# Kernel optimization log

Measured on AMD Instinct MI355X. Metric: run time of the kernel, lower is better.

The kernel has to match this reference:

```python
import jax, jax.numpy as jnp
import numpy as np

N, E, IN, OUT, G = 100000, 800000, 64, 64, 250


def setup_inputs() -> dict:
    key = jax.random.key(0)
    ks = jax.random.split(key, 8)
    x = jax.random.normal(ks[0], (N, IN), dtype=jnp.float32)
    edge_index = jax.random.randint(ks[1], (2, E), 0, N, dtype=jnp.int32)
    edge_weight = jax.random.uniform(ks[2], (E,), dtype=jnp.float32)
    segment_ids = jnp.sort(jax.random.randint(ks[3], (N,), 0, G, dtype=jnp.int32))
    # GCNConv parameters (glorot-ish weights, zero bias as in PyG init)
    W_embed = jax.random.normal(ks[4], (IN, OUT), dtype=jnp.float32) / np.sqrt(IN)
    b_embed = jnp.zeros((OUT,), dtype=jnp.float32)
    W_pool = jax.random.normal(ks[5], (IN, 1), dtype=jnp.float32) / np.sqrt(IN)
    b_pool = jnp.zeros((1,), dtype=jnp.float32)
    return dict(x=x, W_embed=W_embed, b_embed=b_embed, W_pool=W_pool,
                b_pool=b_pool, edge_weight=edge_weight, edge_index=edge_index,
                segment_ids=segment_ids, num_segments=G)


def _gcn(x, W, b, row, col, ew, n):
    """PyG GCNConv: symmetric norm with self-loops already appended."""
    h = x @ W                                            # [N, F]
    deg = jax.ops.segment_sum(ew, col, num_segments=n)   # in-degree incl. self-loops
    dinv = jnp.where(deg > 0, jax.lax.rsqrt(deg), 0.0)
    norm = dinv[row] * ew * dinv[col]                    # [E+N]
    out = jax.ops.segment_sum(norm[:, None] * h[row], col, num_segments=n)
    return out + b


def reference(x, W_embed, b_embed, W_pool, b_pool, edge_weight,
              edge_index, segment_ids, num_segments):
    n = x.shape[0]
    loop = jnp.arange(n, dtype=edge_index.dtype)
    row = jnp.concatenate([edge_index[0], loop])         # add self-loops (w=1)
    col = jnp.concatenate([edge_index[1], loop])
    ew = jnp.concatenate([edge_weight, jnp.ones((n,), edge_weight.dtype)])

    embed = jax.nn.relu(_gcn(x, W_embed, b_embed, row, col, ew, n))  # [N, OUT]
    score = _gcn(x, W_pool, b_pool, row, col, ew, n)[:, 0]           # [N]

    # ragged per-graph softmax over node scores (stable)
    m = jax.ops.segment_max(score, segment_ids, num_segments=num_segments)
    e = jnp.exp(score - m[segment_ids])
    z = jax.ops.segment_sum(e, segment_ids, num_segments=num_segments)
    s = e / z[segment_ids]                               # [N]

    # softmax-weighted pooling of embeddings per graph -> [G, OUT]
    res = jax.ops.segment_sum(s[:, None] * embed, segment_ids,
                              num_segments=num_segments)
    return res
```

## Files before the change

### kernel.cpp

```cpp
#include <hip/hip_runtime.h>
#include <math.h>

#define NIN 64
#define CAP 16
#define GSEG 250
#define POOL_SPLIT 8
#define BND 256
#define CHUNK 2048
#define NBMAX 512

__device__ __forceinline__ float wave_reduce_sum(float v) {
    #pragma unroll
    for (int off = 32; off > 0; off >>= 1) v += __shfl_xor(v, off);
    return v;
}

__device__ __forceinline__ unsigned short f2bf(float f) {
    unsigned int u = __float_as_uint(f);
    u += 0x7FFFu + ((u >> 16) & 1u);
    return (unsigned short)(u >> 16);
}
__device__ __forceinline__ float bf2f(unsigned short h) {
    return __uint_as_float(((unsigned int)h) << 16);
}
__device__ __forceinline__ float bflo(unsigned int u) { return __uint_as_float(u << 16); }
__device__ __forceinline__ float bfhi(unsigned int u) { return __uint_as_float(u & 0xFFFF0000u); }
__device__ __forceinline__ unsigned int pack2bf(float lo, float hi) {
    return (unsigned int)f2bf(lo) | ((unsigned int)f2bf(hi) << 16);
}

__device__ __forceinline__ unsigned int f15enc(float w) {
    unsigned int u = __float_as_uint(w);
    u += 0x0FFFu + ((u >> 13) & 1u);
    int e5 = (int)(u >> 23) - 96;
    if (e5 <= 0) return 0u;
    unsigned int m = (u >> 13) & 0x3FFu;
    if (e5 > 31) { e5 = 31; m = 0x3FFu; }
    return ((unsigned int)e5 << 10) | m;
}
__device__ __forceinline__ float f15dec(unsigned int f) {
    if (f == 0u) return 0.0f;
    return __uint_as_float((((f >> 10) + 96u) << 23) | ((f & 0x3FFu) << 13));
}

__device__ __forceinline__ int wave_excl_scan_int(int x, int lane) {
    int inc = x;
    #pragma unroll
    for (int off = 1; off < 64; off <<= 1) {
        int y = __shfl_up(inc, off);
        if (lane >= off) inc += y;
    }
    return inc - x;
}

__device__ __forceinline__ void scan512_to_lds(const int* __restrict__ src,
                                               int* __restrict__ dst,
                                               int nb, int tid) {
    if (tid < 64) {
        int v[8];
        #pragma unroll
        for (int j = 0; j < 8; ++j) {
            int idx = tid * 8 + j;
            v[j] = (idx < nb) ? src[idx] : 0;
        }
        int loc = 0;
        #pragma unroll
        for (int j = 0; j < 8; ++j) loc += v[j];
        int ex = wave_excl_scan_int(loc, tid);
        int run = ex;
        #pragma unroll
        for (int j = 0; j < 8; ++j) {
            int idx = tid * 8 + j;
            if (idx < nb) { dst[idx] = run; run += v[j]; }
        }
    }
}

__global__ void __launch_bounds__(256)
k_prep(ushort4* __restrict__ x164, const float4* __restrict__ x4,
       float* __restrict__ out, int* __restrict__ gstart, int* __restrict__ gend,
       int* __restrict__ ovf_cnt, const int* __restrict__ col,
       int* __restrict__ ghist, int n, int e, int nb, int nblk) {
    __shared__ int h[NBMAX];
    int tid = threadIdx.x, blk = blockIdx.x;
    int i = blk * 256 + tid;
    int tot = n * (NIN / 4);
    if (i < tot) {
        float4 v = x4[i];
        ushort4 hh;
        hh.x = f2bf(v.x); hh.y = f2bf(v.y); hh.z = f2bf(v.z); hh.w = f2bf(v.w);
        x164[i] = hh;
    }
    if (i < GSEG * NIN) out[i] = 0.0f;
    if (i < GSEG) { gstart[i] = 0; gend[i] = 0; }
    if (i == 0) *ovf_cnt = 0;
    if (blk < nblk) {
        for (int j = tid; j < NBMAX; j += 256) h[j] = 0;
        __syncthreads();
        int base = blk * CHUNK;
        int end = base + CHUNK; if (end > e) end = e;
        for (int j = base + tid; j < end; j += 256) atomicAdd(&h[col[j] >> 8], 1);
        __syncthreads();
        for (int b = tid; b < nb; b += 256) ghist[blk * nb + b] = h[b];
    }
}

__global__ void k_scanA(int* __restrict__ ghist, int* __restrict__ btot,
                        const int* __restrict__ seg, int* __restrict__ gstart,
                        int* __restrict__ gend, int nblk, int nb, int n) {
    int b = blockIdx.x, lane = threadIdx.x;
    int v[8];
    #pragma unroll
    for (int j = 0; j < 8; ++j) {
        int idx = lane * 8 + j;
        v[j] = (idx < nblk) ? ghist[idx * nb + b] : 0;
    }
    int loc = 0;
    #pragma unroll
    for (int j = 0; j < 8; ++j) loc += v[j];
    int ex = wave_excl_scan_int(loc, lane);
    int run = ex;
    #pragma unroll
    for (int j = 0; j < 8; ++j) {
        int idx = lane * 8 + j;
        if (idx < nblk) { int t = v[j]; ghist[idx * nb + b] = run; run += t; }
    }
    if (lane == 63) btot[b] = ex + loc;

    int gsz = gridDim.x * 64;
    for (int i = b * 64 + lane; i < n; i += gsz) {
        int s = seg[i];
        if (i == 0 || seg[i - 1] != s) gstart[s] = i;
        if (i == n - 1 || seg[i + 1] != s) gend[s] = i + 1;
    }
}

__global__ void __launch_bounds__(256)
k_scatter(const int* __restrict__ row, const int* __restrict__ col,
          const float* __restrict__ ew, const int* __restrict__ ghist,
          const int* __restrict__ btot, uint2* __restrict__ bins,
          int e, int nb) {
    __shared__ int h[NBMAX];
    __shared__ int loff[NBMAX];
    __shared__ int gdst[NBMAX];
    __shared__ int bb[NBMAX];
    __shared__ uint2 recs[CHUNK];
    __shared__ unsigned short rb[CHUNK];
    int tid = threadIdx.x, blk = blockIdx.x;
    int base = blk * CHUNK;
    int end = base + CHUNK; if (end > e) end = e;
    int cnt = end - base;

    for (int i = tid; i < NBMAX; i += 256) h[i] = 0;
    __syncthreads();
    for (int i = base + tid; i < end; i += 256) atomicAdd(&h[col[i] >> 8], 1);
    __syncthreads();
    if (tid < 64) {
        int v[8];
        #pragma unroll
        for (int j = 0; j < 8; ++j) {
            int idx = tid * 8 + j;
            v[j] = (idx < nb) ? h[idx] : 0;
        }
        int loc = 0;
        #pragma unroll
        for (int j = 0; j < 8; ++j) loc += v[j];
        int ex = wave_excl_scan_int(loc, tid);
        int run = ex;
        #pragma unroll
        for (int j = 0; j < 8; ++j) {
            int idx = tid * 8 + j;
            if (idx < nb) { loff[idx] = run; run += v[j]; }
        }
    }
    scan512_to_lds(btot, bb, nb, tid);
    __syncthreads();
    for (int b = tid; b < nb; b += 256) gdst[b] = bb[b] + ghist[blk * nb + b];
    for (int i = tid; i < NBMAX; i += 256) h[i] = 0;
    __syncthreads();
    for (int i = base + tid; i < end; i += 256) {
        int c = col[i];
        int b = c >> 8;
        uint2 rec;
        rec.x = (unsigned int)row[i];
        rec.y = ((unsigned int)(c & (BND - 1)) << 15) | f15enc(ew[i]);
        int k = atomicAdd(&h[b], 1);
        int idx = loff[b] + k;
        recs[idx] = rec;
        rb[idx] = (unsigned short)b;
    }
    __syncthreads();
    for (int i = tid; i < cnt; i += 256) {
        int b = rb[i];
        bins[(size_t)gdst[b] + (i - loff[b])] = recs[i];
    }
}

__global__ void __launch_bounds__(256)
k_build(const uint2* __restrict__ bins, const int* __restrict__ btot,
        unsigned int* __restrict__ ell, float* __restrict__ deg,
        int* __restrict__ cnt, int2* __restrict__ ovf, int* __restrict__ ovf_cnt,
        float* __restrict__ aggf, int n, int nb) {
    int b = blockIdx.x;
    int c0 = b << 8;
    int nn = n - c0; if (nn > BND) nn = BND;
    __shared__ unsigned int tile[BND * CAP];
    __shared__ float sdeg[BND];
    __shared__ int scnt[BND];
    __shared__ int bb[NBMAX];
    __shared__ int ovl[BND];
    __shared__ int novloc;
    int tid = threadIdx.x;
    sdeg[tid] = 0.0f; scnt[tid] = 0;
    if (tid == 0) novloc = 0;
    for (int i = tid; i < BND * CAP; i += 256) tile[i] = 0u;
    scan512_to_lds(btot, bb, nb, tid);
    __syncthreads();
    int s0 = bb[b], tot = btot[b];
    for (int i = tid; i < tot; i += 256) {
        uint2 rec = bins[(size_t)s0 + i];
        int cl = (int)((rec.y >> 15) & (BND - 1));
        unsigned int w15 = rec.y & 0x7FFFu;
        atomicAdd(&sdeg[cl], f15dec(w15));
        int slot = atomicAdd(&scnt[cl], 1);
        unsigned int p = (rec.x << 15) | w15;
        if (slot < CAP) {
            tile[cl * CAP + slot] = p;
        } else {
            int oi = atomicAdd(ovf_cnt, 1);
            ovf[oi] = make_int2(c0 + cl, (int)p);
        }
    }
    __syncthreads();
    for (int i = tid; i < nn * CAP; i += 256)
        ell[(size_t)c0 * CAP + i] = tile[i];
    if (tid < nn) {
        deg[c0 + tid] = sdeg[tid] + 1.0f;
        cnt[c0 + tid] = scnt[tid];
        if (scnt[tid] > CAP) { int k = atomicAdd(&novloc, 1); ovl[k] = tid; }
    }
    __syncthreads();
    int nov = novloc;
    for (int k = 0; k < nov; ++k) {
        if (tid < NIN) aggf[(size_t)(c0 + ovl[k]) * NIN + tid] = 0.0f;
    }
}

__global__ void k_ovf(const int2* __restrict__ ovf, const int* __restrict__ ovf_cnt,
                      const float* __restrict__ deg, const ushort* __restrict__ x16,
                      float* __restrict__ aggf) {
    int nov = *ovf_cnt;
    int wid = (int)((blockIdx.x * (size_t)blockDim.x + threadIdx.x) >> 6);
    int lane = threadIdx.x & 63;
    int nw = (int)((gridDim.x * (size_t)blockDim.x) >> 6);
    for (int i = wid; i < nov; i += nw) {
        int2 ov = ovf[i];
        int c = ov.x;
        unsigned int p = (unsigned int)ov.y;
        int r = (int)(p >> 15);
        float w = f15dec(p & 0x7FFFu) * rsqrtf(deg[r]) * rsqrtf(deg[c]);
        atomicAdd(&aggf[(size_t)c * NIN + lane], w * bf2f(x16[(size_t)r * NIN + lane]));
    }
}

__global__ void __launch_bounds__(256)
k_gather(const ushort* __restrict__ x16, const float* __restrict__ deg,
         const int* __restrict__ cnt, const unsigned int* __restrict__ ell,
         const float* __restrict__ aggf, ushort* __restrict__ agg16,
         const float* __restrict__ Wp, const float* __restrict__ bp,
         float* __restrict__ score, int n) {
    int wid = (int)((blockIdx.x * (size_t)blockDim.x + threadIdx.x) >> 6);
    int lane = threadIdx.x & 63;
    int o = lane >> 3, l = lane & 7;
    int c0 = wid * 8;
    if (c0 >= n) return;
    int c = c0 + o;
    bool valid = c < n;
    int cc = valid ? c : (n - 1);

    int cr = cnt[cc];
    int m = valid ? (cr < CAP ? cr : CAP) : 0;
    float di = rsqrtf(deg[cc]);

    const uint2* ell2 = (const uint2*)ell;
    uint2 pe = ell2[(size_t)cc * 8 + l];
    int pr0 = (int)(pe.x >> 15);
    float pw0 = f15dec(pe.x & 0x7FFFu) * rsqrtf(deg[pr0]);
    int pr1 = (int)(pe.y >> 15);
    float pw1 = f15dec(pe.y & 0x7FFFu) * rsqrtf(deg[pr1]);

    const uint4* xr4 = (const uint4*)x16;
    uint4 xs = xr4[(size_t)cc * 8 + l];
    float a0 = di * bflo(xs.x), a1 = di * bfhi(xs.x);
    float a2 = di * bflo(xs.y), a3 = di * bfhi(xs.y);
    float a4 = di * bflo(xs.z), a5 = di * bfhi(xs.z);
    float a6 = di * bflo(xs.w), a7 = di * bfhi(xs.w);

    int base = lane & 56;
    #pragma unroll
    for (int k = 0; k < 8; ++k) {
        int rk = __shfl((k & 1) ? pr1 : pr0, base + (k >> 1));
        float wk = __shfl((k & 1) ? pw1 : pw0, base + (k >> 1));
        bool v = k < m;
        int r = v ? rk : 0;
        float w = v ? wk : 0.0f;
        uint4 xr = xr4[(size_t)r * 8 + l];
        a0 = fmaf(w, bflo(xr.x), a0); a1 = fmaf(w, bfhi(xr.x), a1);
        a2 = fmaf(w, bflo(xr.y), a2); a3 = fmaf(w, bfhi(xr.y), a3);
        a4 = fmaf(w, bflo(xr.z), a4); a5 = fmaf(w, bfhi(xr.z), a5);
        a6 = fmaf(w, bflo(xr.w), a6); a7 = fmaf(w, bfhi(xr.w), a7);
    }
    if (__any(m > 8)) {
        #pragma unroll
        for (int k = 8; k < CAP; ++k) {
            int rk = __shfl((k & 1) ? pr1 : pr0, base + (k >> 1));
            float wk = __shfl((k & 1) ? pw1 : pw0, base + (k >> 1));
            bool v = k < m;
            int r = v ? rk : 0;
            float w = v ? wk : 0.0f;
            uint4 xr = xr4[(size_t)r * 8 + l];
            a0 = fmaf(w, bflo(xr.x), a0); a1 = fmaf(w, bfhi(xr.x), a1);
            a2 = fmaf(w, bflo(xr.y), a2); a3 = fmaf(w, bfhi(xr.y), a3);
            a4 = fmaf(w, bflo(xr.z), a4); a5 = fmaf(w, bfhi(xr.z), a5);
            a6 = fmaf(w, bflo(xr.w), a6); a7 = fmaf(w, bfhi(xr.w), a7);
        }
    }
    a0 *= di; a1 *= di; a2 *= di; a3 *= di;
    a4 *= di; a5 *= di; a6 *= di; a7 *= di;

    if (valid && cr > CAP) {
        const float4* af4 = (const float4*)aggf;
        float4 f0 = af4[(size_t)cc * 16 + 2 * l];
        float4 f1 = af4[(size_t)cc * 16 + 2 * l + 1];
        a0 += f0.x; a1 += f0.y; a2 += f0.z; a3 += f0.w;
        a4 += f1.x; a5 += f1.y; a6 += f1.z; a7 += f1.w;
    }

    if (valid) {
        uint4 ho;
        ho.x = pack2bf(a0, a1); ho.y = pack2bf(a2, a3);
        ho.z = pack2bf(a4, a5); ho.w = pack2bf(a6, a7);
        ((uint4*)agg16)[(size_t)cc * 8 + l] = ho;
    }

    const float4* wp4 = (const float4*)Wp;
    float4 w0 = wp4[2 * l], w1 = wp4[2 * l + 1];
    float part = a0 * w0.x + a1 * w0.y + a2 * w0.z + a3 * w0.w
               + a4 * w1.x + a5 * w1.y + a6 * w1.z + a7 * w1.w;
    part += __shfl_xor(part, 1);
    part += __shfl_xor(part, 2);
    part += __shfl_xor(part, 4);
    if (l == 0 && valid) score[c] = part + bp[0];
}

#define WLOAD(i) float4 wq##i = make_float4(We[(4*(i)+0)*NIN+lane], We[(4*(i)+1)*NIN+lane], \
                                            We[(4*(i)+2)*NIN+lane], We[(4*(i)+3)*NIN+lane]);
#define WSTEP(i) { float4 av = *(const float4*)&als[wv][4*(i)]; \
    e0 = fmaf(av.x, wq##i.x, e0); e1 = fmaf(av.y, wq##i.y, e1); \
    e2 = fmaf(av.z, wq##i.z, e2); e3 = fmaf(av.w, wq##i.w, e3); }

__global__ void __launch_bounds__(256)
k_pool(const ushort* __restrict__ agg16, const float* __restrict__ score,
       const float* __restrict__ We, const float* __restrict__ be,
       const int* __restrict__ gstart, const int* __restrict__ gend,
       float* __restrict__ out) {
    int g = blockIdx.x / POOL_SPLIT;
    int p = blockIdx.x % POOL_SPLIT;
    int tid = threadIdx.x;
    int wv = tid >> 6, lane = tid & 63;
    int s = gstart[g], e = gend[g];

    __shared__ float red[4];
    __shared__ float bc;

    float mx = -3.402823466e38f;
    for (int i = s + tid; i < e; i += 256) mx = fmaxf(mx, score[i]);
    #pragma unroll
    for (int off = 32; off > 0; off >>= 1) mx = fmaxf(mx, __shfl_xor(mx, off));
    if (lane == 0) red[wv] = mx;
    __syncthreads();
    if (tid == 0) bc = fmaxf(fmaxf(red[0], red[1]), fmaxf(red[2], red[3]));
    __syncthreads();
    float m = bc;
    __syncthreads();

    float sm = 0.0f;
    for (int i = s + tid; i < e; i += 256) sm += __expf(score[i] - m);
    sm = wave_reduce_sum(sm);
    if (lane == 0) red[wv] = sm;
    __syncthreads();
    if (tid == 0) bc = red[0] + red[1] + red[2] + red[3];
    __syncthreads();
    float invz = (bc > 0.0f) ? 1.0f / bc : 0.0f;

    WLOAD(0) WLOAD(1) WLOAD(2) WLOAD(3) WLOAD(4) WLOAD(5) WLOAD(6) WLOAD(7)
    WLOAD(8) WLOAD(9) WLOAD(10) WLOAD(11) WLOAD(12) WLOAD(13) WLOAD(14) WLOAD(15)
    float bj = be[lane];

    __shared__ float als[4][NIN];
    __shared__ float part[4][NIN];

    const int stride = POOL_SPLIT * 4;
    int n = s + p * 4 + wv;
    float acc = 0.0f;

    float a_cur = 0.0f, sw_cur = 0.0f;
    if (n < e) {
        a_cur = bf2f(agg16[(size_t)n * NIN + lane]);
        sw_cur = __expf(score[n] - m) * invz;
    }
    while (n < e) {
        int nn = n + stride;
        bool vn = nn < e;
        int ni = vn ? nn : n;
        float a_nxt = bf2f(agg16[(size_t)ni * NIN + lane]);
        float sw_nxt = __expf(score[ni] - m) * invz;

        als[wv][lane] = a_cur;
        float e0 = bj, e1 = 0.0f, e2 = 0.0f, e3 = 0.0f;
        WSTEP(0) WSTEP(1) WSTEP(2) WSTEP(3) WSTEP(4) WSTEP(5) WSTEP(6) WSTEP(7)
        WSTEP(8) WSTEP(9) WSTEP(10) WSTEP(11) WSTEP(12) WSTEP(13) WSTEP(14) WSTEP(15)
        float emb = fmaxf(e0 + e1 + e2 + e3, 0.0f);
        acc = fmaf(sw_cur, emb, acc);

        a_cur = a_nxt; sw_cur = sw_nxt;
        n = nn;
    }
    part[wv][lane] = acc;
    __syncthreads();
    if (wv == 0) {
        float r = part[0][lane] + part[1][lane] + part[2][lane] + part[3][lane];
        atomicAdd(&out[(size_t)g * NIN + lane], r);
    }
}

extern "C" void kernel_launch(void* const* d_in, const int* in_sizes, int n_in,
                              void* d_out, int out_size, void* d_ws, size_t ws_size,
                              hipStream_t stream) {
    const float* x  = (const float*)d_in[0];
    const float* We = (const float*)d_in[1];
    const float* be = (const float*)d_in[2];
    const float* Wp = (const float*)d_in[3];
    const float* bp = (const float*)d_in[4];
    const float* ew = (const float*)d_in[5];
    const int* eidx = (const int*)d_in[6];
    const int* seg  = (const int*)d_in[7];

    int N = in_sizes[0] / NIN;
    int E = in_sizes[5];
    const int* row = eidx;
    const int* col = eidx + E;
    int nb   = (N + BND - 1) / BND;
    int nblk = (E + CHUNK - 1) / CHUNK;

    char* w = (char*)d_ws;
    auto alloc = [&](size_t bytes) {
        char* p = w;
        w += (bytes + 255) & ~(size_t)255;
        return p;
    };
    float*          aggf    = (float*)alloc((size_t)N * NIN * sizeof(float));
    unsigned short* x16     = (unsigned short*)alloc((size_t)N * NIN * sizeof(short));
    unsigned short* agg16   = (unsigned short*)alloc((size_t)N * NIN * sizeof(short));
    float*          deg     = (float*)alloc((size_t)N * sizeof(float));
    int*            cnt     = (int*)  alloc((size_t)N * sizeof(int));
    unsigned int*   ell     = (unsigned int*)alloc((size_t)N * CAP * sizeof(unsigned int));
    uint2*          bins    = (uint2*)alloc((size_t)E * sizeof(uint2));
    int*            ghist   = (int*)  alloc((size_t)nblk * nb * sizeof(int));
    int*            btot    = (int*)  alloc((size_t)nb * sizeof(int));
    int2*           ovf     = (int2*) alloc((size_t)(E / 4) * sizeof(int2));
    int*            ovf_cnt = (int*)  alloc(256);
    float*          score   = (float*)alloc((size_t)N * sizeof(float));
    int*            gstart  = (int*)  alloc(GSEG * sizeof(int));
    int*            gend    = (int*)  alloc(GSEG * sizeof(int));
    float* out = (float*)d_out;

    int b = 256;
    int g_prep   = (N * (NIN / 4) + b - 1) / b;
    int nwaves   = (N + 7) / 8;
    int g_gather = (nwaves + 3) / 4;

    k_prep<<<g_prep, b, 0, stream>>>((ushort4*)x16, (const float4*)x, out, gstart,
                                     gend, ovf_cnt, col, ghist, N, E, nb, nblk);
    k_scanA<<<nb, 64, 0, stream>>>(ghist, btot, seg, gstart, gend, nblk, nb, N);
    k_scatter<<<nblk, b, 0, stream>>>(row, col, ew, ghist, btot, bins, E, nb);
    k_build<<<nb, b, 0, stream>>>(bins, btot, ell, deg, cnt, ovf, ovf_cnt, aggf, N, nb);
    k_ovf<<<64, b, 0, stream>>>(ovf, ovf_cnt, deg, x16, aggf);
    k_gather<<<g_gather, b, 0, stream>>>(x16, deg, cnt, ell, aggf, agg16, Wp, bp, score, N);
    k_pool<<<GSEG * POOL_SPLIT, b, 0, stream>>>(agg16, score, We, be, gstart, gend, out);
}
```

Measured before the change: 89.08 us.

## Fuse bucket build, overflow handling and gather into one LDS-tiled kernel

Merges k_build, k_ovf and k_gather into a single kernel, k_bg. It keeps each bucket's ELL tile and overflow edges in LDS and gathers directly from there, so the global ELL, count and fp32 overflow buffers are no longer needed. Degree is now computed with global atomics inside the scan kernel, and the symmetric normalisation is folded into the edge weight during scatter. Buckets shrink to 128 nodes to fit the larger tile. In exchange there are fewer gather blocks, more serial work per block, and overflow edges beyond 256 per bucket would be silently dropped.

```diff
diff --git a/kernel.cpp b/kernel.cpp
--- a/kernel.cpp
+++ b/kernel.cpp
@@ -5,9 +5,12 @@
 #define CAP 16
 #define GSEG 250
 #define POOL_SPLIT 8
-#define BND 256
+#define BND 128
+#define BSH 7
 #define CHUNK 2048
-#define NBMAX 512
+#define NBMAX 1024
+#define OVRMAX 256
+#define TS 17
 
 __device__ __forceinline__ float wave_reduce_sum(float v) {
     #pragma unroll
@@ -53,24 +56,23 @@
     return inc - x;
 }
 
-__device__ __forceinline__ void scan512_to_lds(const int* __restrict__ src,
-                                               int* __restrict__ dst,
-                                               int nb, int tid) {
+__device__ __forceinline__ void scan_btot(const int* __restrict__ src,
+                                          int* dst, int nb, int tid) {
     if (tid < 64) {
-        int v[8];
-        #pragma unroll
-        for (int j = 0; j < 8; ++j) {
-            int idx = tid * 8 + j;
+        int v[16];
+        #pragma unroll
+        for (int j = 0; j < 16; ++j) {
+            int idx = tid * 16 + j;
             v[j] = (idx < nb) ? src[idx] : 0;
         }
         int loc = 0;
         #pragma unroll
-        for (int j = 0; j < 8; ++j) loc += v[j];
+        for (int j = 0; j < 16; ++j) loc += v[j];
         int ex = wave_excl_scan_int(loc, tid);
         int run = ex;
         #pragma unroll
-        for (int j = 0; j < 8; ++j) {
-            int idx = tid * 8 + j;
+        for (int j = 0; j < 16; ++j) {
+            int idx = tid * 16 + j;
             if (idx < nb) { dst[idx] = run; run += v[j]; }
         }
     }
@@ -79,7 +81,7 @@
 __global__ void __launch_bounds__(256)
 k_prep(ushort4* __restrict__ x164, const float4* __restrict__ x4,
        float* __restrict__ out, int* __restrict__ gstart, int* __restrict__ gend,
-       int* __restrict__ ovf_cnt, const int* __restrict__ col,
+       float* __restrict__ deg, const int* __restrict__ col,
        int* __restrict__ ghist, int n, int e, int nb, int nblk) {
     __shared__ int h[NBMAX];
     int tid = threadIdx.x, blk = blockIdx.x;
@@ -91,44 +93,51 @@
         hh.x = f2bf(v.x); hh.y = f2bf(v.y); hh.z = f2bf(v.z); hh.w = f2bf(v.w);
         x164[i] = hh;
     }
+    if (i < n) deg[i] = 0.0f;
     if (i < GSEG * NIN) out[i] = 0.0f;
     if (i < GSEG) { gstart[i] = 0; gend[i] = 0; }
-    if (i == 0) *ovf_cnt = 0;
     if (blk < nblk) {
         for (int j = tid; j < NBMAX; j += 256) h[j] = 0;
         __syncthreads();
         int base = blk * CHUNK;
         int end = base + CHUNK; if (end > e) end = e;
-        for (int j = base + tid; j < end; j += 256) atomicAdd(&h[col[j] >> 8], 1);
+        for (int j = base + tid; j < end; j += 256) atomicAdd(&h[col[j] >> BSH], 1);
         __syncthreads();
         for (int b = tid; b < nb; b += 256) ghist[blk * nb + b] = h[b];
     }
 }
 
-__global__ void k_scanA(int* __restrict__ ghist, int* __restrict__ btot,
-                        const int* __restrict__ seg, int* __restrict__ gstart,
-                        int* __restrict__ gend, int nblk, int nb, int n) {
-    int b = blockIdx.x, lane = threadIdx.x;
-    int v[8];
-    #pragma unroll
-    for (int j = 0; j < 8; ++j) {
-        int idx = lane * 8 + j;
-        v[j] = (idx < nblk) ? ghist[idx * nb + b] : 0;
-    }
-    int loc = 0;
-    #pragma unroll
-    for (int j = 0; j < 8; ++j) loc += v[j];
-    int ex = wave_excl_scan_int(loc, lane);
-    int run = ex;
-    #pragma unroll
-    for (int j = 0; j < 8; ++j) {
-        int idx = lane * 8 + j;
-        if (idx < nblk) { int t = v[j]; ghist[idx * nb + b] = run; run += t; }
-    }
-    if (lane == 63) btot[b] = ex + loc;
-
-    int gsz = gridDim.x * 64;
-    for (int i = b * 64 + lane; i < n; i += gsz) {
+__global__ void __launch_bounds__(256)
+k_scanA(int* __restrict__ ghist, int* __restrict__ btot,
+        const int* __restrict__ seg, int* __restrict__ gstart,
+        int* __restrict__ gend, const int* __restrict__ col,
+        const float* __restrict__ ew, float* __restrict__ deg,
+        int nblk, int nb, int n, int e) {
+    int tid = threadIdx.x;
+    int b = blockIdx.x;
+    if (tid < 64) {
+        int lane = tid;
+        int v[8];
+        #pragma unroll
+        for (int j = 0; j < 8; ++j) {
+            int idx = lane * 8 + j;
+            v[j] = (idx < nblk) ? ghist[idx * nb + b] : 0;
+        }
+        int loc = 0;
+        #pragma unroll
+        for (int j = 0; j < 8; ++j) loc += v[j];
+        int ex = wave_excl_scan_int(loc, lane);
+        int run = ex;
+        #pragma unroll
+        for (int j = 0; j < 8; ++j) {
+            int idx = lane * 8 + j;
+            if (idx < nblk) { int t = v[j]; ghist[idx * nb + b] = run; run += t; }
+        }
+        if (lane == 63) btot[b] = ex + loc;
+    }
+    int gsz = gridDim.x * 256;
+    for (int i = b * 256 + tid; i < e; i += gsz) atomicAdd(&deg[col[i]], ew[i]);
+    for (int i = b * 256 + tid; i < n; i += gsz) {
         int s = seg[i];
         if (i == 0 || seg[i - 1] != s) gstart[s] = i;
         if (i == n - 1 || seg[i + 1] != s) gend[s] = i + 1;
@@ -137,9 +146,9 @@
 
 __global__ void __launch_bounds__(256)
 k_scatter(const int* __restrict__ row, const int* __restrict__ col,
-          const float* __restrict__ ew, const int* __restrict__ ghist,
-          const int* __restrict__ btot, uint2* __restrict__ bins,
-          int e, int nb) {
+          const float* __restrict__ ew, const float* __restrict__ deg,
+          const int* __restrict__ ghist, const int* __restrict__ btot,
+          uint2* __restrict__ bins, int e, int nb) {
     __shared__ int h[NBMAX];
     __shared__ int loff[NBMAX];
     __shared__ int gdst[NBMAX];
@@ -149,170 +158,125 @@
     int tid = threadIdx.x, blk = blockIdx.x;
     int base = blk * CHUNK;
     int end = base + CHUNK; if (end > e) end = e;
-    int cnt = end - base;
+    int cntc = end - base;
 
     for (int i = tid; i < NBMAX; i += 256) h[i] = 0;
     __syncthreads();
-    for (int i = base + tid; i < end; i += 256) atomicAdd(&h[col[i] >> 8], 1);
+    for (int i = base + tid; i < end; i += 256) atomicAdd(&h[col[i] >> BSH], 1);
     __syncthreads();
     if (tid < 64) {
-        int v[8];
-        #pragma unroll
-        for (int j = 0; j < 8; ++j) {
-            int idx = tid * 8 + j;
+        int v[16];
+        #pragma unroll
+        for (int j = 0; j < 16; ++j) {
+            int idx = tid * 16 + j;
             v[j] = (idx < nb) ? h[idx] : 0;
         }
         int loc = 0;
         #pragma unroll
-        for (int j = 0; j < 8; ++j) loc += v[j];
+        for (int j = 0; j < 16; ++j) loc += v[j];
         int ex = wave_excl_scan_int(loc, tid);
         int run = ex;
         #pragma unroll
-        for (int j = 0; j < 8; ++j) {
-            int idx = tid * 8 + j;
+        for (int j = 0; j < 16; ++j) {
+            int idx = tid * 16 + j;
             if (idx < nb) { loff[idx] = run; run += v[j]; }
         }
     }
-    scan512_to_lds(btot, bb, nb, tid);
+    scan_btot(btot, bb, nb, tid);
     __syncthreads();
     for (int b = tid; b < nb; b += 256) gdst[b] = bb[b] + ghist[blk * nb + b];
     for (int i = tid; i < NBMAX; i += 256) h[i] = 0;
     __syncthreads();
     for (int i = base + tid; i < end; i += 256) {
-        int c = col[i];
-        int b = c >> 8;
+        int c = col[i], r = row[i];
+        int b = c >> BSH;
+        float w = ew[i] * rsqrtf(deg[r] + 1.0f) * rsqrtf(deg[c] + 1.0f);
         uint2 rec;
-        rec.x = (unsigned int)row[i];
-        rec.y = ((unsigned int)(c & (BND - 1)) << 15) | f15enc(ew[i]);
+        rec.x = (unsigned int)r;
+        rec.y = ((unsigned int)(c & (BND - 1)) << 15) | f15enc(w);
         int k = atomicAdd(&h[b], 1);
         int idx = loff[b] + k;
         recs[idx] = rec;
         rb[idx] = (unsigned short)b;
     }
     __syncthreads();
-    for (int i = tid; i < cnt; i += 256) {
+    for (int i = tid; i < cntc; i += 256) {
         int b = rb[i];
         bins[(size_t)gdst[b] + (i - loff[b])] = recs[i];
     }
 }
 
 __global__ void __launch_bounds__(256)
-k_build(const uint2* __restrict__ bins, const int* __restrict__ btot,
-        unsigned int* __restrict__ ell, float* __restrict__ deg,
-        int* __restrict__ cnt, int2* __restrict__ ovf, int* __restrict__ ovf_cnt,
-        float* __restrict__ aggf, int n, int nb) {
-    int b = blockIdx.x;
-    int c0 = b << 8;
-    int nn = n - c0; if (nn > BND) nn = BND;
-    __shared__ unsigned int tile[BND * CAP];
-    __shared__ float sdeg[BND];
+k_bg(const uint2* __restrict__ bins, const int* __restrict__ btot,
+     const float* __restrict__ deg, const ushort* __restrict__ x16,
+     ushort* __restrict__ agg16, const float* __restrict__ Wp,
+     const float* __restrict__ bp, float* __restrict__ score, int n, int nb) {
+    __shared__ unsigned int tile[BND * TS];
     __shared__ int scnt[BND];
     __shared__ int bb[NBMAX];
-    __shared__ int ovl[BND];
-    __shared__ int novloc;
+    __shared__ int ovr_cl[OVRMAX];
+    __shared__ unsigned int ovr_rec[OVRMAX];
+    __shared__ int ovn;
     int tid = threadIdx.x;
-    sdeg[tid] = 0.0f; scnt[tid] = 0;
-    if (tid == 0) novloc = 0;
-    for (int i = tid; i < BND * CAP; i += 256) tile[i] = 0u;
-    scan512_to_lds(btot, bb, nb, tid);
-    __syncthreads();
+    int b = blockIdx.x;
+    int c0 = b << BSH;
+
+    if (tid < BND) scnt[tid] = 0;
+    if (tid == 0) ovn = 0;
+    scan_btot(btot, bb, nb, tid);
+    __syncthreads();
+
     int s0 = bb[b], tot = btot[b];
     for (int i = tid; i < tot; i += 256) {
         uint2 rec = bins[(size_t)s0 + i];
         int cl = (int)((rec.y >> 15) & (BND - 1));
-        unsigned int w15 = rec.y & 0x7FFFu;
-        atomicAdd(&sdeg[cl], f15dec(w15));
+        unsigned int p = (rec.x << 15) | (rec.y & 0x7FFFu);
         int slot = atomicAdd(&scnt[cl], 1);
-        unsigned int p = (rec.x << 15) | w15;
         if (slot < CAP) {
-            tile[cl * CAP + slot] = p;
+            tile[cl * TS + slot] = p;
         } else {
-            int oi = atomicAdd(ovf_cnt, 1);
-            ovf[oi] = make_int2(c0 + cl, (int)p);
-        }
-    }
-    __syncthreads();
-    for (int i = tid; i < nn * CAP; i += 256)
-        ell[(size_t)c0 * CAP + i] = tile[i];
-    if (tid < nn) {
-        deg[c0 + tid] = sdeg[tid] + 1.0f;
-        cnt[c0 + tid] = scnt[tid];
-        if (scnt[tid] > CAP) { int k = atomicAdd(&novloc, 1); ovl[k] = tid; }
-    }
-    __syncthreads();
-    int nov = novloc;
-    for (int k = 0; k < nov; ++k) {
-        if (tid < NIN) aggf[(size_t)(c0 + ovl[k]) * NIN + tid] = 0.0f;
-    }
-}
-
-__global__ void k_ovf(const int2* __restrict__ ovf, const int* __restrict__ ovf_cnt,
-                      const float* __restrict__ deg, const ushort* __restrict__ x16,
-                      float* __restrict__ aggf) {
-    int nov = *ovf_cnt;
-    int wid = (int)((blockIdx.x * (size_t)blockDim.x + threadIdx.x) >> 6);
-    int lane = threadIdx.x & 63;
-    int nw = (int)((gridDim.x * (size_t)blockDim.x) >> 6);
-    for (int i = wid; i < nov; i += nw) {
-        int2 ov = ovf[i];
-        int c = ov.x;
-        unsigned int p = (unsigned int)ov.y;
-        int r = (int)(p >> 15);
-        float w = f15dec(p & 0x7FFFu) * rsqrtf(deg[r]) * rsqrtf(deg[c]);
-        atomicAdd(&aggf[(size_t)c * NIN + lane], w * bf2f(x16[(size_t)r * NIN + lane]));
-    }
-}
-
-__global__ void __launch_bounds__(256)
-k_gather(const ushort* __restrict__ x16, const float* __restrict__ deg,
-         const int* __restrict__ cnt, const unsigned int* __restrict__ ell,
-         const float* __restrict__ aggf, ushort* __restrict__ agg16,
-         const float* __restrict__ Wp, const float* __restrict__ bp,
-         float* __restrict__ score, int n) {
-    int wid = (int)((blockIdx.x * (size_t)blockDim.x + threadIdx.x) >> 6);
-    int lane = threadIdx.x & 63;
+            int oi = atomicAdd(&ovn, 1);
+            if (oi < OVRMAX) { ovr_cl[oi] = cl; ovr_rec[oi] = p; }
+        }
+    }
+    __syncthreads();
+
+    int lane = tid & 63, wv = tid >> 6;
     int o = lane >> 3, l = lane & 7;
-    int c0 = wid * 8;
-    if (c0 >= n) return;
-    int c = c0 + o;
-    bool valid = c < n;
-    int cc = valid ? c : (n - 1);
-
-    int cr = cnt[cc];
-    int m = valid ? (cr < CAP ? cr : CAP) : 0;
-    float di = rsqrtf(deg[cc]);
-
-    const uint2* ell2 = (const uint2*)ell;
-    uint2 pe = ell2[(size_t)cc * 8 + l];
-    int pr0 = (int)(pe.x >> 15);
-    float pw0 = f15dec(pe.x & 0x7FFFu) * rsqrtf(deg[pr0]);
-    int pr1 = (int)(pe.y >> 15);
-    float pw1 = f15dec(pe.y & 0x7FFFu) * rsqrtf(deg[pr1]);
-
+    const float4* wp4 = (const float4*)Wp;
+    float4 w0 = wp4[2 * l], w1 = wp4[2 * l + 1];
+    float bp0 = bp[0];
     const uint4* xr4 = (const uint4*)x16;
-    uint4 xs = xr4[(size_t)cc * 8 + l];
-    float a0 = di * bflo(xs.x), a1 = di * bfhi(xs.x);
-    float a2 = di * bflo(xs.y), a3 = di * bfhi(xs.y);
-    float a4 = di * bflo(xs.z), a5 = di * bfhi(xs.z);
-    float a6 = di * bflo(xs.w), a7 = di * bfhi(xs.w);
-
-    int base = lane & 56;
+    int nov = ovn;
+
     #pragma unroll
-    for (int k = 0; k < 8; ++k) {
-        int rk = __shfl((k & 1) ? pr1 : pr0, base + (k >> 1));
-        float wk = __shfl((k & 1) ? pw1 : pw0, base + (k >> 1));
-        bool v = k < m;
-        int r = v ? rk : 0;
-        float w = v ? wk : 0.0f;
-        uint4 xr = xr4[(size_t)r * 8 + l];
-        a0 = fmaf(w, bflo(xr.x), a0); a1 = fmaf(w, bfhi(xr.x), a1);
-        a2 = fmaf(w, bflo(xr.y), a2); a3 = fmaf(w, bfhi(xr.y), a3);
-        a4 = fmaf(w, bflo(xr.z), a4); a5 = fmaf(w, bfhi(xr.z), a5);
-        a6 = fmaf(w, bflo(xr.w), a6); a7 = fmaf(w, bfhi(xr.w), a7);
-    }
-    if (__any(m > 8)) {
-        #pragma unroll
-        for (int k = 8; k < CAP; ++k) {
+    for (int it = 0; it < BND / 32; ++it) {
+        int bl = it * 32 + wv * 8;
+        int nl = bl + o;
+        int c = c0 + nl;
+        bool valid = c < n;
+        int cc = valid ? c : (n - 1);
+        int cr = scnt[nl];
+        int m = valid ? (cr < CAP ? cr : CAP) : 0;
+        float di = rsqrtf(deg[cc] + 1.0f);
+
+        unsigned int u0 = tile[nl * TS + 2 * l];
+        unsigned int u1 = tile[nl * TS + 2 * l + 1];
+        int pr0 = (int)(u0 >> 15);
+        float pw0 = f15dec(u0 & 0x7FFFu);
+        int pr1 = (int)(u1 >> 15);
+        float pw1 = f15dec(u1 & 0x7FFFu);
+
+        uint4 xs = xr4[(size_t)cc * 8 + l];
+        float s2 = di * di;
+        float a0 = s2 * bflo(xs.x), a1 = s2 * bfhi(xs.x);
+        float a2 = s2 * bflo(xs.y), a3 = s2 * bfhi(xs.y);
+        float a4 = s2 * bflo(xs.z), a5 = s2 * bfhi(xs.z);
+        float a6 = s2 * bflo(xs.w), a7 = s2 * bfhi(xs.w);
+
+        int base = lane & 56;
+        #pragma unroll
+        for (int k = 0; k < 8; ++k) {
             int rk = __shfl((k & 1) ? pr1 : pr0, base + (k >> 1));
             float wk = __shfl((k & 1) ? pw1 : pw0, base + (k >> 1));
             bool v = k < m;
@@ -324,33 +288,49 @@
             a4 = fmaf(w, bflo(xr.z), a4); a5 = fmaf(w, bfhi(xr.z), a5);
             a6 = fmaf(w, bflo(xr.w), a6); a7 = fmaf(w, bfhi(xr.w), a7);
         }
-    }
-    a0 *= di; a1 *= di; a2 *= di; a3 *= di;
-    a4 *= di; a5 *= di; a6 *= di; a7 *= di;
-
-    if (valid && cr > CAP) {
-        const float4* af4 = (const float4*)aggf;
-        float4 f0 = af4[(size_t)cc * 16 + 2 * l];
-        float4 f1 = af4[(size_t)cc * 16 + 2 * l + 1];
-        a0 += f0.x; a1 += f0.y; a2 += f0.z; a3 += f0.w;
-        a4 += f1.x; a5 += f1.y; a6 += f1.z; a7 += f1.w;
-    }
-
-    if (valid) {
-        uint4 ho;
-        ho.x = pack2bf(a0, a1); ho.y = pack2bf(a2, a3);
-        ho.z = pack2bf(a4, a5); ho.w = pack2bf(a6, a7);
-        ((uint4*)agg16)[(size_t)cc * 8 + l] = ho;
-    }
-
-    const float4* wp4 = (const float4*)Wp;
-    float4 w0 = wp4[2 * l], w1 = wp4[2 * l + 1];
-    float part = a0 * w0.x + a1 * w0.y + a2 * w0.z + a3 * w0.w
-               + a4 * w1.x + a5 * w1.y + a6 * w1.z + a7 * w1.w;
-    part += __shfl_xor(part, 1);
-    part += __shfl_xor(part, 2);
-    part += __shfl_xor(part, 4);
-    if (l == 0 && valid) score[c] = part + bp[0];
+        if (__any(m > 8)) {
+            #pragma unroll
+            for (int k = 8; k < CAP; ++k) {
+                int rk = __shfl((k & 1) ? pr1 : pr0, base + (k >> 1));
+                float wk = __shfl((k & 1) ? pw1 : pw0, base + (k >> 1));
+                bool v = k < m;
+                int r = v ? rk : 0;
+                float w = v ? wk : 0.0f;
+                uint4 xr = xr4[(size_t)r * 8 + l];
+                a0 = fmaf(w, bflo(xr.x), a0); a1 = fmaf(w, bfhi(xr.x), a1);
+                a2 = fmaf(w, bflo(xr.y), a2); a3 = fmaf(w, bfhi(xr.y), a3);
+                a4 = fmaf(w, bflo(xr.z), a4); a5 = fmaf(w, bfhi(xr.z), a5);
+                a6 = fmaf(w, bflo(xr.w), a6); a7 = fmaf(w, bfhi(xr.w), a7);
+            }
+        }
+        for (int i = 0; i < nov; ++i) {
+            int cl = ovr_cl[i];
+            if (cl >= bl && cl < bl + 8) {
+                unsigned int rec = ovr_rec[i];
+                int r = (int)(rec >> 15);
+                float wvv = f15dec(rec & 0x7FFFu);
+                float wm = (cl == nl) ? wvv : 0.0f;
+                uint4 xr = xr4[(size_t)r * 8 + l];
+                a0 = fmaf(wm, bflo(xr.x), a0); a1 = fmaf(wm, bfhi(xr.x), a1);
+                a2 = fmaf(wm, bflo(xr.y), a2); a3 = fmaf(wm, bfhi(xr.y), a3);
+                a4 = fmaf(wm, bflo(xr.z), a4); a5 = fmaf(wm, bfhi(xr.z), a5);
+                a6 = fmaf(wm, bflo(xr.w), a6); a7 = fmaf(wm, bfhi(xr.w), a7);
+            }
+        }
+
+        if (valid) {
+            uint4 ho;
+            ho.x = pack2bf(a0, a1); ho.y = pack2bf(a2, a3);
+            ho.z = pack2bf(a4, a5); ho.w = pack2bf(a6, a7);
+            ((uint4*)agg16)[(size_t)cc * 8 + l] = ho;
+        }
+        float part = a0 * w0.x + a1 * w0.y + a2 * w0.z + a3 * w0.w
+                   + a4 * w1.x + a5 * w1.y + a6 * w1.z + a7 * w1.w;
+        part += __shfl_xor(part, 1);
+        part += __shfl_xor(part, 2);
+        part += __shfl_xor(part, 4);
+        if (l == 0 && valid) score[c] = part + bp0;
+    }
 }
 
 #define WLOAD(i) float4 wq##i = make_float4(We[(4*(i)+0)*NIN+lane], We[(4*(i)+1)*NIN+lane], \
@@ -459,33 +439,25 @@
         w += (bytes + 255) & ~(size_t)255;
         return p;
     };
-    float*          aggf    = (float*)alloc((size_t)N * NIN * sizeof(float));
-    unsigned short* x16     = (unsigned short*)alloc((size_t)N * NIN * sizeof(short));
-    unsigned short* agg16   = (unsigned short*)alloc((size_t)N * NIN * sizeof(short));
-    float*          deg     = (float*)alloc((size_t)N * sizeof(float));
-    int*            cnt     = (int*)  alloc((size_t)N * sizeof(int));
-    unsigned int*   ell     = (unsigned int*)alloc((size_t)N * CAP * sizeof(unsigned int));
-    uint2*          bins    = (uint2*)alloc((size_t)E * sizeof(uint2));
-    int*            ghist   = (int*)  alloc((size_t)nblk * nb * sizeof(int));
-    int*            btot    = (int*)  alloc((size_t)nb * sizeof(int));
-    int2*           ovf     = (int2*) alloc((size_t)(E / 4) * sizeof(int2));
-    int*            ovf_cnt = (int*)  alloc(256);
-    float*          score   = (float*)alloc((size_t)N * sizeof(float));
-    int*            gstart  = (int*)  alloc(GSEG * sizeof(int));
-    int*            gend    = (int*)  alloc(GSEG * sizeof(int));
+    unsigned short* x16    = (unsigned short*)alloc((size_t)N * NIN * sizeof(short));
+    unsigned short* agg16  = (unsigned short*)alloc((size_t)N * NIN * sizeof(short));
+    float*          deg    = (float*)alloc((size_t)N * sizeof(float));
+    uint2*          bins   = (uint2*)alloc((size_t)E * sizeof(uint2));
+    int*            ghist  = (int*)  alloc((size_t)nblk * nb * sizeof(int));
+    int*            btot   = (int*)  alloc((size_t)nb * sizeof(int));
+    float*          score  = (float*)alloc((size_t)N * sizeof(float));
+    int*            gstart = (int*)  alloc(GSEG * sizeof(int));
+    int*            gend   = (int*)  alloc(GSEG * sizeof(int));
     float* out = (float*)d_out;
 
     int b = 256;
-    int g_prep   = (N * (NIN / 4) + b - 1) / b;
-    int nwaves   = (N + 7) / 8;
-    int g_gather = (nwaves + 3) / 4;
+    int g_prep = (N * (NIN / 4) + b - 1) / b;
 
     k_prep<<<g_prep, b, 0, stream>>>((ushort4*)x16, (const float4*)x, out, gstart,
-                                     gend, ovf_cnt, col, ghist, N, E, nb, nblk);
-    k_scanA<<<nb, 64, 0, stream>>>(ghist, btot, seg, gstart, gend, nblk, nb, N);
-    k_scatter<<<nblk, b, 0, stream>>>(row, col, ew, ghist, btot, bins, E, nb);
-    k_build<<<nb, b, 0, stream>>>(bins, btot, ell, deg, cnt, ovf, ovf_cnt, aggf, N, nb);
-    k_ovf<<<64, b, 0, stream>>>(ovf, ovf_cnt, deg, x16, aggf);
-    k_gather<<<g_gather, b, 0, stream>>>(x16, deg, cnt, ell, aggf, agg16, Wp, bp, score, N);
+                                     gend, deg, col, ghist, N, E, nb, nblk);
+    k_scanA<<<nb, b, 0, stream>>>(ghist, btot, seg, gstart, gend, col, ew, deg,
+                                  nblk, nb, N, E);
+    k_scatter<<<nblk, b, 0, stream>>>(row, col, ew, deg, ghist, btot, bins, E, nb);
+    k_bg<<<nb, b, 0, stream>>>(bins, btot, deg, x16, agg16, Wp, bp, score, N, nb);
     k_pool<<<GSEG * POOL_SPLIT, b, 0, stream>>>(agg16, score, We, be, gstart, gend, out);
 }
```

Measured after the change: 129.3 us. 1.45x slower.

## Fold overflow edge handling into gather via per-bucket overflow lists

Applied to the files above, without the earlier changes.

Edges beyond each node's ELL capacity are no longer pushed to a global list by global atomics. k_build now keeps them in a small shared-memory list per 256-node bucket and writes that list out. k_gather then walks its bucket's overflow entries and accumulates the matching ones directly. This removes the k_ovf launch, the float aggregation buffer with its global atomic adds, and the extra read in gather. The cost is that every gather wave scans all overflow entries of its bucket. Overflow beyond 128 entries per bucket is silently dropped, which risks wrong results on skewed degree distributions.

```diff
diff --git a/kernel.cpp b/kernel.cpp
--- a/kernel.cpp
+++ b/kernel.cpp
@@ -8,6 +8,7 @@
 #define BND 256
 #define CHUNK 2048
 #define NBMAX 512
+#define OVR 128
 
 __device__ __forceinline__ float wave_reduce_sum(float v) {
     #pragma unroll
@@ -53,9 +54,8 @@
     return inc - x;
 }
 
-__device__ __forceinline__ void scan512_to_lds(const int* __restrict__ src,
-                                               int* __restrict__ dst,
-                                               int nb, int tid) {
+__device__ __forceinline__ void scan_btot(const int* __restrict__ src,
+                                          int* dst, int nb, int tid) {
     if (tid < 64) {
         int v[8];
         #pragma unroll
@@ -79,8 +79,8 @@
 __global__ void __launch_bounds__(256)
 k_prep(ushort4* __restrict__ x164, const float4* __restrict__ x4,
        float* __restrict__ out, int* __restrict__ gstart, int* __restrict__ gend,
-       int* __restrict__ ovf_cnt, const int* __restrict__ col,
-       int* __restrict__ ghist, int n, int e, int nb, int nblk) {
+       const int* __restrict__ col, int* __restrict__ ghist,
+       int n, int e, int nb, int nblk) {
     __shared__ int h[NBMAX];
     int tid = threadIdx.x, blk = blockIdx.x;
     int i = blk * 256 + tid;
@@ -93,7 +93,6 @@
     }
     if (i < GSEG * NIN) out[i] = 0.0f;
     if (i < GSEG) { gstart[i] = 0; gend[i] = 0; }
-    if (i == 0) *ovf_cnt = 0;
     if (blk < nblk) {
         for (int j = tid; j < NBMAX; j += 256) h[j] = 0;
         __syncthreads();
@@ -149,7 +148,7 @@
     int tid = threadIdx.x, blk = blockIdx.x;
     int base = blk * CHUNK;
     int end = base + CHUNK; if (end > e) end = e;
-    int cnt = end - base;
+    int cntc = end - base;
 
     for (int i = tid; i < NBMAX; i += 256) h[i] = 0;
     __syncthreads();
@@ -173,16 +172,16 @@
             if (idx < nb) { loff[idx] = run; run += v[j]; }
         }
     }
-    scan512_to_lds(btot, bb, nb, tid);
+    scan_btot(btot, bb, nb, tid);
     __syncthreads();
     for (int b = tid; b < nb; b += 256) gdst[b] = bb[b] + ghist[blk * nb + b];
     for (int i = tid; i < NBMAX; i += 256) h[i] = 0;
     __syncthreads();
     for (int i = base + tid; i < end; i += 256) {
-        int c = col[i];
+        int c = col[i], r = row[i];
         int b = c >> 8;
         uint2 rec;
-        rec.x = (unsigned int)row[i];
+        rec.x = (unsigned int)r;
         rec.y = ((unsigned int)(c & (BND - 1)) << 15) | f15enc(ew[i]);
         int k = atomicAdd(&h[b], 1);
         int idx = loff[b] + k;
@@ -190,7 +189,7 @@
         rb[idx] = (unsigned short)b;
     }
     __syncthreads();
-    for (int i = tid; i < cnt; i += 256) {
+    for (int i = tid; i < cntc; i += 256) {
         int b = rb[i];
         bins[(size_t)gdst[b] + (i - loff[b])] = recs[i];
     }
@@ -199,22 +198,22 @@
 __global__ void __launch_bounds__(256)
 k_build(const uint2* __restrict__ bins, const int* __restrict__ btot,
         unsigned int* __restrict__ ell, float* __restrict__ deg,
-        int* __restrict__ cnt, int2* __restrict__ ovf, int* __restrict__ ovf_cnt,
-        float* __restrict__ aggf, int n, int nb) {
-    int b = blockIdx.x;
-    int c0 = b << 8;
-    int nn = n - c0; if (nn > BND) nn = BND;
+        int* __restrict__ cnt, int* __restrict__ ovfc, int2* __restrict__ ovfe,
+        int n, int nb) {
     __shared__ unsigned int tile[BND * CAP];
     __shared__ float sdeg[BND];
     __shared__ int scnt[BND];
     __shared__ int bb[NBMAX];
-    __shared__ int ovl[BND];
-    __shared__ int novloc;
+    __shared__ int2 sovf[OVR];
+    __shared__ int sovn;
     int tid = threadIdx.x;
+    int b = blockIdx.x;
+    int c0 = b << 8;
+    int nn = n - c0; if (nn > BND) nn = BND;
     sdeg[tid] = 0.0f; scnt[tid] = 0;
-    if (tid == 0) novloc = 0;
+    if (tid == 0) sovn = 0;
     for (int i = tid; i < BND * CAP; i += 256) tile[i] = 0u;
-    scan512_to_lds(btot, bb, nb, tid);
+    scan_btot(btot, bb, nb, tid);
     __syncthreads();
     int s0 = bb[b], tot = btot[b];
     for (int i = tid; i < tot; i += 256) {
@@ -227,8 +226,8 @@
         if (slot < CAP) {
             tile[cl * CAP + slot] = p;
         } else {
-            int oi = atomicAdd(ovf_cnt, 1);
-            ovf[oi] = make_int2(c0 + cl, (int)p);
+            int oi = atomicAdd(&sovn, 1);
+            if (oi < OVR) sovf[oi] = make_int2(((int)rec.x << 8) | cl, (int)w15);
         }
     }
     __syncthreads();
@@ -237,46 +236,25 @@
     if (tid < nn) {
         deg[c0 + tid] = sdeg[tid] + 1.0f;
         cnt[c0 + tid] = scnt[tid];
-        if (scnt[tid] > CAP) { int k = atomicAdd(&novloc, 1); ovl[k] = tid; }
-    }
-    __syncthreads();
-    int nov = novloc;
-    for (int k = 0; k < nov; ++k) {
-        if (tid < NIN) aggf[(size_t)(c0 + ovl[k]) * NIN + tid] = 0.0f;
-    }
-}
-
-__global__ void k_ovf(const int2* __restrict__ ovf, const int* __restrict__ ovf_cnt,
-                      const float* __restrict__ deg, const ushort* __restrict__ x16,
-                      float* __restrict__ aggf) {
-    int nov = *ovf_cnt;
-    int wid = (int)((blockIdx.x * (size_t)blockDim.x + threadIdx.x) >> 6);
-    int lane = threadIdx.x & 63;
-    int nw = (int)((gridDim.x * (size_t)blockDim.x) >> 6);
-    for (int i = wid; i < nov; i += nw) {
-        int2 ov = ovf[i];
-        int c = ov.x;
-        unsigned int p = (unsigned int)ov.y;
-        int r = (int)(p >> 15);
-        float w = f15dec(p & 0x7FFFu) * rsqrtf(deg[r]) * rsqrtf(deg[c]);
-        atomicAdd(&aggf[(size_t)c * NIN + lane], w * bf2f(x16[(size_t)r * NIN + lane]));
-    }
+    }
+    int nov = sovn < OVR ? sovn : OVR;
+    if (tid == 0) ovfc[b] = nov;
+    for (int i = tid; i < nov; i += 256) ovfe[(size_t)b * OVR + i] = sovf[i];
 }
 
 __global__ void __launch_bounds__(256)
 k_gather(const ushort* __restrict__ x16, const float* __restrict__ deg,
          const int* __restrict__ cnt, const unsigned int* __restrict__ ell,
-         const float* __restrict__ aggf, ushort* __restrict__ agg16,
-         const float* __restrict__ Wp, const float* __restrict__ bp,
-         float* __restrict__ score, int n) {
-    int wid = (int)((blockIdx.x * (size_t)blockDim.x + threadIdx.x) >> 6);
-    int lane = threadIdx.x & 63;
+         const int* __restrict__ ovfc, const int2* __restrict__ ovfe,
+         ushort* __restrict__ agg16, const float* __restrict__ Wp,
+         const float* __restrict__ bp, float* __restrict__ score, int n) {
+    int tid = threadIdx.x, blk = blockIdx.x;
+    int lane = tid & 63, wv = tid >> 6;
     int o = lane >> 3, l = lane & 7;
-    int c0 = wid * 8;
-    if (c0 >= n) return;
-    int c = c0 + o;
+    int c = blk * 32 + wv * 8 + o;
     bool valid = c < n;
     int cc = valid ? c : (n - 1);
+    int b = blk >> 3;
 
     int cr = cnt[cc];
     int m = valid ? (cr < CAP ? cr : CAP) : 0;
@@ -325,16 +303,22 @@
             a6 = fmaf(w, bflo(xr.w), a6); a7 = fmaf(w, bfhi(xr.w), a7);
         }
     }
+    int novb = ovfc[b];
+    int nl = cc & (BND - 1);
+    for (int i = 0; i < novb; ++i) {
+        int2 ent = ovfe[(size_t)b * OVR + i];
+        int cl = ent.x & (BND - 1);
+        int r = ent.x >> 8;
+        bool mine = (cl == nl) && valid;
+        float wm = mine ? f15dec((unsigned int)ent.y) * rsqrtf(deg[r]) : 0.0f;
+        uint4 xr = xr4[(size_t)r * 8 + l];
+        a0 = fmaf(wm, bflo(xr.x), a0); a1 = fmaf(wm, bfhi(xr.x), a1);
+        a2 = fmaf(wm, bflo(xr.y), a2); a3 = fmaf(wm, bfhi(xr.y), a3);
+        a4 = fmaf(wm, bflo(xr.z), a4); a5 = fmaf(wm, bfhi(xr.z), a5);
+        a6 = fmaf(wm, bflo(xr.w), a6); a7 = fmaf(wm, bfhi(xr.w), a7);
+    }
     a0 *= di; a1 *= di; a2 *= di; a3 *= di;
     a4 *= di; a5 *= di; a6 *= di; a7 *= di;
-
-    if (valid && cr > CAP) {
-        const float4* af4 = (const float4*)aggf;
-        float4 f0 = af4[(size_t)cc * 16 + 2 * l];
-        float4 f1 = af4[(size_t)cc * 16 + 2 * l + 1];
-        a0 += f0.x; a1 += f0.y; a2 += f0.z; a3 += f0.w;
-        a4 += f1.x; a5 += f1.y; a6 += f1.z; a7 += f1.w;
-    }
 
     if (valid) {
         uint4 ho;
@@ -342,7 +326,6 @@
         ho.z = pack2bf(a4, a5); ho.w = pack2bf(a6, a7);
         ((uint4*)agg16)[(size_t)cc * 8 + l] = ho;
     }
-
     const float4* wp4 = (const float4*)Wp;
     float4 w0 = wp4[2 * l], w1 = wp4[2 * l + 1];
     float part = a0 * w0.x + a1 * w0.y + a2 * w0.z + a3 * w0.w
@@ -459,33 +442,31 @@
         w += (bytes + 255) & ~(size_t)255;
         return p;
     };
-    float*          aggf    = (float*)alloc((size_t)N * NIN * sizeof(float));
-    unsigned short* x16     = (unsigned short*)alloc((size_t)N * NIN * sizeof(short));
-    unsigned short* agg16   = (unsigned short*)alloc((size_t)N * NIN * sizeof(short));
-    float*          deg     = (float*)alloc((size_t)N * sizeof(float));
-    int*            cnt     = (int*)  alloc((size_t)N * sizeof(int));
-    unsigned int*   ell     = (unsigned int*)alloc((size_t)N * CAP * sizeof(unsigned int));
-    uint2*          bins    = (uint2*)alloc((size_t)E * sizeof(uint2));
-    int*            ghist   = (int*)  alloc((size_t)nblk * nb * sizeof(int));
-    int*            btot    = (int*)  alloc((size_t)nb * sizeof(int));
-    int2*           ovf     = (int2*) alloc((size_t)(E / 4) * sizeof(int2));
-    int*            ovf_cnt = (int*)  alloc(256);
-    float*          score   = (float*)alloc((size_t)N * sizeof(float));
-    int*            gstart  = (int*)  alloc(GSEG * sizeof(int));
-    int*            gend    = (int*)  alloc(GSEG * sizeof(int));
+    unsigned short* x16    = (unsigned short*)alloc((size_t)N * NIN * sizeof(short));
+    unsigned short* agg16  = (unsigned short*)alloc((size_t)N * NIN * sizeof(short));
+    float*          deg    = (float*)alloc((size_t)N * sizeof(float));
+    int*            cnt    = (int*)  alloc((size_t)N * sizeof(int));
+    unsigned int*   ell    = (unsigned int*)alloc((size_t)N * CAP * sizeof(unsigned int));
+    uint2*          bins   = (uint2*)alloc((size_t)E * sizeof(uint2));
+    int*            ghist  = (int*)  alloc((size_t)nblk * nb * sizeof(int));
+    int*            btot   = (int*)  alloc((size_t)nb * sizeof(int));
+    int*            ovfc   = (int*)  alloc((size_t)nb * sizeof(int));
+    int2*           ovfe   = (int2*) alloc((size_t)nb * OVR * sizeof(int2));
+    float*          score  = (float*)alloc((size_t)N * sizeof(float));
+    int*            gstart = (int*)  alloc(GSEG * sizeof(int));
+    int*            gend   = (int*)  alloc(GSEG * sizeof(int));
     float* out = (float*)d_out;
 
     int b = 256;
     int g_prep   = (N * (NIN / 4) + b - 1) / b;
-    int nwaves   = (N + 7) / 8;
-    int g_gather = (nwaves + 3) / 4;
+    int g_gather = (N + 31) / 32;
 
     k_prep<<<g_prep, b, 0, stream>>>((ushort4*)x16, (const float4*)x, out, gstart,
-                                     gend, ovf_cnt, col, ghist, N, E, nb, nblk);
+                                     gend, col, ghist, N, E, nb, nblk);
     k_scanA<<<nb, 64, 0, stream>>>(ghist, btot, seg, gstart, gend, nblk, nb, N);
     k_scatter<<<nblk, b, 0, stream>>>(row, col, ew, ghist, btot, bins, E, nb);
-    k_build<<<nb, b, 0, stream>>>(bins, btot, ell, deg, cnt, ovf, ovf_cnt, aggf, N, nb);
-    k_ovf<<<64, b, 0, stream>>>(ovf, ovf_cnt, deg, x16, aggf);
-    k_gather<<<g_gather, b, 0, stream>>>(x16, deg, cnt, ell, aggf, agg16, Wp, bp, score, N);
+    k_build<<<nb, b, 0, stream>>>(bins, btot, ell, deg, cnt, ovfc, ovfe, N, nb);
+    k_gather<<<g_gather, b, 0, stream>>>(x16, deg, cnt, ell, ovfc, ovfe,
+                                         agg16, Wp, bp, score, N);
     k_pool<<<GSEG * POOL_SPLIT, b, 0, stream>>>(agg16, score, We, be, gstart, gend, out);
 }
```

After: 84.85 us. 1.05x faster.
